# Performance work log

Measured on AMD Instinct MI355X. Metric: run time of the kernel, lower is better.

## Reference

```python
import jax, jax.numpy as jnp
import numpy as np

N = 100000      # nodes
E = 3200000     # edges (avg degree 32)
IN, HID, OUT = 512, 256, 64
K = 10
ALPHA = 0.1


def setup_inputs() -> dict:
    key = jax.random.key(0)
    k1, k2, k3, k4 = jax.random.split(key, 4)
    x = jax.random.normal(k1, (N, IN), dtype=jnp.float32)
    edge_index = jax.random.randint(k2, (2, E), 0, N, dtype=jnp.int64)
    # MLP params (Kaiming-ish scaling)
    W1 = jax.random.normal(k3, (IN, HID), dtype=jnp.float32) / np.sqrt(IN)
    b1 = jnp.zeros((HID,), dtype=jnp.float32)
    W2 = jax.random.normal(k4, (HID, OUT), dtype=jnp.float32) / np.sqrt(HID)
    b2 = jnp.zeros((OUT,), dtype=jnp.float32)
    # GPR_prop PPR init: temp[k] = alpha*(1-alpha)^k, temp[K] = (1-alpha)^K
    ks = np.arange(K + 1)
    temp = ALPHA * (1.0 - ALPHA) ** ks
    temp[-1] = (1.0 - ALPHA) ** K
    temp = jnp.asarray(temp, dtype=jnp.float32)
    return {"x": x, "edge_index": edge_index, "W1": W1, "b1": b1,
            "W2": W2, "b2": b2, "temp": temp}


def reference(x, edge_index, W1, b1, W2, b2, temp):
    # MLP front-end (eval mode: dropout = identity)
    h = jax.nn.relu(x @ W1 + b1)
    h = h @ W2 + b2                                  # [N, OUT]

    # gcn_norm with self-loops: A_hat = D^{-1/2} (A + I) D^{-1/2}
    loop = jnp.arange(N, dtype=edge_index.dtype)
    src = jnp.concatenate([edge_index[0], loop])      # [E+N]
    dst = jnp.concatenate([edge_index[1], loop])      # [E+N]
    deg = jax.ops.segment_sum(jnp.ones_like(dst, dtype=h.dtype), dst,
                              num_segments=N)
    dis = jnp.where(deg > 0, jax.lax.rsqrt(deg), 0.0)
    norm = (dis[src] * dis[dst])[:, None]             # [E+N, 1]

    # GPR propagation: out = sum_k temp[k] * A_hat^k h
    def step(carry, gamma):
        hk, acc = carry
        hk = jax.ops.segment_sum(norm * hk[src], dst, num_segments=N)
        return (hk, acc + gamma * hk), None

    (_, out), _ = jax.lax.scan(step, (h, temp[0] * h), temp[1:])
    return out
```

## Files before the change

kernel.cpp:

```cpp
#include <hip/hip_runtime.h>

#define NN 100000
#define NE 3200000
#define DIN 512
#define DHID 256
#define DOUT 64
#define KPROP 10

typedef _Float16 f16;
typedef _Float16 f16x8 __attribute__((ext_vector_type(8)));
typedef _Float16 f16x4 __attribute__((ext_vector_type(4)));
typedef float f32x4 __attribute__((ext_vector_type(4)));

__global__ void detect_i64(const int* __restrict__ ei, int* __restrict__ flag) {
  int lane = threadIdx.x;
  int ok = 1;
  for (int i = lane; i < 512; i += 64)
    if (ei[2 * i + 1] != 0) ok = 0;
  ok = __all(ok);
  if (lane == 0) *flag = ok;
}

__global__ void zero_cnt(int* __restrict__ cnt) {
  int g = blockIdx.x * blockDim.x + threadIdx.x;
  if (g < NN) cnt[g] = 0;
}

__global__ void count_deg(const int* __restrict__ ei, const int* __restrict__ flag,
                          int* __restrict__ cnt, int* __restrict__ rank) {
  int g = blockIdx.x * blockDim.x + threadIdx.x;
  int e0 = g * 4;
  if (e0 >= NE) return;
  int is64 = *flag;
  int d0, d1, d2, d3;
  if (is64) {
    int4 a = *(const int4*)&ei[2 * (size_t)NE + 2 * (size_t)e0];
    int4 b = *(const int4*)&ei[2 * (size_t)NE + 2 * (size_t)e0 + 4];
    d0 = a.x; d1 = a.z; d2 = b.x; d3 = b.z;
  } else {
    int4 a = *(const int4*)&ei[(size_t)NE + e0];
    d0 = a.x; d1 = a.y; d2 = a.z; d3 = a.w;
  }
  int4 rk;
  rk.x = atomicAdd(&cnt[d0], 1);
  rk.y = atomicAdd(&cnt[d1], 1);
  rk.z = atomicAdd(&cnt[d2], 1);
  rk.w = atomicAdd(&cnt[d3], 1);
  *(int4*)&rank[e0] = rk;
}

__global__ void scan1(const int* __restrict__ cnt, int* __restrict__ rs,
                      int* __restrict__ bsum) {
  __shared__ int tmp[1024];
  int t = threadIdx.x;
  int g = blockIdx.x * 1024 + t;
  int v = (g < NN) ? cnt[g] : 0;
  tmp[t] = v;
  __syncthreads();
  for (int off = 1; off < 1024; off <<= 1) {
    int y = (t >= off) ? tmp[t - off] : 0;
    __syncthreads();
    tmp[t] += y;
    __syncthreads();
  }
  if (g < NN) rs[g] = tmp[t] - v;
  if (t == 1023) bsum[blockIdx.x] = tmp[t];
}

__global__ void scan2(int* __restrict__ bsum, int nb) {
  if (blockIdx.x == 0 && threadIdx.x == 0) {
    int s = 0;
    for (int i = 0; i < nb; i++) { int v = bsum[i]; bsum[i] = s; s += v; }
  }
}

__global__ void scan3_and_dis(int* __restrict__ rs, const int* __restrict__ bsum,
                              const int* __restrict__ cnt, float* __restrict__ dis) {
  int g = blockIdx.x * blockDim.x + threadIdx.x;
  if (g < NN) {
    rs[g] = rs[g] + bsum[g >> 10];
    dis[g] = rsqrtf((float)(cnt[g] + 1));
  }
}

__global__ void fill_csr(const int* __restrict__ ei, const int* __restrict__ flag,
                         const int* __restrict__ rs, const int* __restrict__ rank,
                         int* __restrict__ col) {
  int g = blockIdx.x * blockDim.x + threadIdx.x;
  int e0 = g * 4;
  if (e0 >= NE) return;
  int is64 = *flag;
  int s[4], d[4];
  if (is64) {
    int4 a = *(const int4*)&ei[2 * (size_t)NE + 2 * (size_t)e0];
    int4 b = *(const int4*)&ei[2 * (size_t)NE + 2 * (size_t)e0 + 4];
    d[0] = a.x; d[1] = a.z; d[2] = b.x; d[3] = b.z;
    int4 c = *(const int4*)&ei[2 * (size_t)e0];
    int4 e = *(const int4*)&ei[2 * (size_t)e0 + 4];
    s[0] = c.x; s[1] = c.z; s[2] = e.x; s[3] = e.z;
  } else {
    int4 a = *(const int4*)&ei[(size_t)NE + e0];
    d[0] = a.x; d[1] = a.y; d[2] = a.z; d[3] = a.w;
    int4 c = *(const int4*)&ei[e0];
    s[0] = c.x; s[1] = c.y; s[2] = c.z; s[3] = c.w;
  }
  int4 rk = *(const int4*)&rank[e0];
  int rka[4] = { rk.x, rk.y, rk.z, rk.w };
  #pragma unroll
  for (int j = 0; j < 4; j++)
    col[rs[d[j]] + rka[j]] = s[j];
}

__global__ void cvt_weights(const float* __restrict__ W1, const float* __restrict__ W2,
                            f16* __restrict__ W1t, f16* __restrict__ W2t) {
  int g = blockIdx.x * 256 + threadIdx.x;
  if (g < DIN * DHID) {
    int k = g >> 8, n = g & 255;
    W1t[(size_t)n * DIN + k] = (f16)W1[g];
  }
  if (g < DHID * DOUT) {
    int k = g >> 6, n = g & 63;
    W2t[(size_t)n * DHID + k] = (f16)W2[g];
  }
}

__global__ __launch_bounds__(256) void mlp_mfma(
    const float* __restrict__ x, const f16* __restrict__ W1t,
    const float* __restrict__ b1, const f16* __restrict__ W2t,
    const float* __restrict__ b2, const float* __restrict__ temp,
    const float* __restrict__ dis, f16* __restrict__ h, f16* __restrict__ zs)
{
  __shared__ __align__(16) char smraw[2 * 64 * 136 * 2];
  f16* xsb = (f16*)smraw;
  f16* h1s = (f16*)smraw;
  int t = threadIdx.x;
  int lane = t & 63;
  int w = t >> 6;
  int n0 = blockIdx.x * 64;
  int r15 = lane & 15;
  int g4 = lane >> 4;
  int nbase = w * 64;
  int srow = t >> 5, sc4 = t & 31;

  f32x4 acc[4][4];
  #pragma unroll
  for (int nt = 0; nt < 4; nt++) {
    float bv = b1[nbase + nt * 16 + r15];
    #pragma unroll
    for (int mt = 0; mt < 4; mt++) acc[mt][nt] = (f32x4){bv, bv, bv, bv};
  }

  float4 ld[8];
  #pragma unroll
  for (int it = 0; it < 8; it++) {
    int row = srow + it * 8;
    int gr = n0 + row;
    ld[it] = (gr < NN) ? *(const float4*)&x[(size_t)gr * DIN + sc4 * 4]
                       : make_float4(0.f, 0.f, 0.f, 0.f);
  }
  #pragma unroll
  for (int it = 0; it < 8; it++) {
    int row = srow + it * 8;
    f16x4 hv = { (f16)ld[it].x, (f16)ld[it].y, (f16)ld[it].z, (f16)ld[it].w };
    *(f16x4*)&xsb[row * 136 + sc4 * 4] = hv;
  }
  __syncthreads();

  for (int c = 0; c < 4; c++) {
    int cur = c & 1;
    if (c < 3) {
      #pragma unroll
      for (int it = 0; it < 8; it++) {
        int row = srow + it * 8;
        int gr = n0 + row;
        ld[it] = (gr < NN)
            ? *(const float4*)&x[(size_t)gr * DIN + (c + 1) * 128 + sc4 * 4]
            : make_float4(0.f, 0.f, 0.f, 0.f);
      }
    }
    int k0 = c * 128;
    const f16* xs = xsb + cur * 8704;
    #pragma unroll
    for (int ks = 0; ks < 4; ks++) {
      int kk = ks * 32 + g4 * 8;
      f16x8 a[4], b[4];
      #pragma unroll
      for (int mt = 0; mt < 4; mt++)
        a[mt] = *(const f16x8*)&xs[(mt * 16 + r15) * 136 + kk];
      #pragma unroll
      for (int nt = 0; nt < 4; nt++)
        b[nt] = *(const f16x8*)&W1t[(size_t)(nbase + nt * 16 + r15) * DIN + k0 + kk];
      #pragma unroll
      for (int mt = 0; mt < 4; mt++)
        #pragma unroll
        for (int nt = 0; nt < 4; nt++)
          acc[mt][nt] = __builtin_amdgcn_mfma_f32_16x16x32_f16(a[mt], b[nt], acc[mt][nt], 0, 0, 0);
    }
    if (c < 3) {
      #pragma unroll
      for (int it = 0; it < 8; it++) {
        int row = srow + it * 8;
        f16x4 hv = { (f16)ld[it].x, (f16)ld[it].y, (f16)ld[it].z, (f16)ld[it].w };
        *(f16x4*)&xsb[(cur ^ 1) * 8704 + row * 136 + sc4 * 4] = hv;
      }
    }
    __syncthreads();
  }

  #pragma unroll
  for (int mt = 0; mt < 4; mt++)
    #pragma unroll
    for (int nt = 0; nt < 4; nt++)
      #pragma unroll
      for (int r = 0; r < 4; r++) {
        float v = fmaxf(acc[mt][nt][r], 0.f);
        h1s[(mt * 16 + g4 * 4 + r) * 264 + nbase + nt * 16 + r15] = (f16)v;
      }
  __syncthreads();

  f32x4 acc2[4];
  #pragma unroll
  for (int nt = 0; nt < 4; nt++) {
    float bv = b2[nt * 16 + r15];
    acc2[nt] = (f32x4){bv, bv, bv, bv};
  }
  #pragma unroll
  for (int ks = 0; ks < 8; ks++) {
    int kk = ks * 32 + g4 * 8;
    f16x8 a2 = *(const f16x8*)&h1s[(w * 16 + r15) * 264 + kk];
    #pragma unroll
    for (int nt = 0; nt < 4; nt++) {
      f16x8 bf = *(const f16x8*)&W2t[(size_t)(nt * 16 + r15) * DHID + kk];
      acc2[nt] = __builtin_amdgcn_mfma_f32_16x16x32_f16(a2, bf, acc2[nt], 0, 0, 0);
    }
  }
  float tK = temp[KPROP];
  #pragma unroll
  for (int r = 0; r < 4; r++) {
    int node = n0 + w * 16 + g4 * 4 + r;
    if (node < NN) {
      float dv = dis[node] * tK;
      #pragma unroll
      for (int nt = 0; nt < 4; nt++) {
        int colv = nt * 16 + r15;
        float v = acc2[nt][r];
        h[(size_t)node * DOUT + colv] = (f16)v;
        zs[(size_t)node * DOUT + colv] = (f16)(dv * v);
      }
    }
  }
}

__global__ __launch_bounds__(256) void prop_horner(
    const f16* __restrict__ zs, f16* __restrict__ zsn, const f16* __restrict__ h,
    float* __restrict__ out, const int* __restrict__ rs, const int* __restrict__ cnt,
    const int* __restrict__ col, const float* __restrict__ dis,
    const float* __restrict__ temp, int kidx, int final_step)
{
  int w = blockIdx.x * 4 + (threadIdx.x >> 6);
  int lane = threadIdx.x & 63;
  if (w >= NN) return;
  int q = lane >> 3;
  int s8 = lane & 7;

  float dd = dis[w];
  float gk = temp[kidx];
  f16x8 zself = *(const f16x8*)&zs[(size_t)w * DOUT + s8 * 8];
  f16x8 hs = *(const f16x8*)&h[(size_t)w * DOUT + s8 * 8];

  float acc[8];
  #pragma unroll
  for (int f = 0; f < 8; f++) acc[f] = 0.f;

  int beg = rs[w], n = cnt[w];
  const int* cp = col + beg;

  int e = 0;
  for (; e + 32 <= n; e += 32) {
    int c0 = cp[e + q];
    int c1 = cp[e + 8 + q];
    int c2 = cp[e + 16 + q];
    int c3 = cp[e + 24 + q];
    f16x8 g0 = *(const f16x8*)&zs[(size_t)c0 * DOUT + s8 * 8];
    f16x8 g1 = *(const f16x8*)&zs[(size_t)c1 * DOUT + s8 * 8];
    f16x8 g2 = *(const f16x8*)&zs[(size_t)c2 * DOUT + s8 * 8];
    f16x8 g3 = *(const f16x8*)&zs[(size_t)c3 * DOUT + s8 * 8];
    #pragma unroll
    for (int f = 0; f < 8; f++) acc[f] += (float)g0[f];
    #pragma unroll
    for (int f = 0; f < 8; f++) acc[f] += (float)g1[f];
    #pragma unroll
    for (int f = 0; f < 8; f++) acc[f] += (float)g2[f];
    #pragma unroll
    for (int f = 0; f < 8; f++) acc[f] += (float)g3[f];
  }
  for (; e + 8 <= n; e += 8) {
    int c0 = cp[e + q];
    f16x8 g0 = *(const f16x8*)&zs[(size_t)c0 * DOUT + s8 * 8];
    #pragma unroll
    for (int f = 0; f < 8; f++) acc[f] += (float)g0[f];
  }
  if (e < n) {
    int rem = n - e;
    int qq = q < rem ? q : rem - 1;
    int c0 = cp[e + qq];
    f16x8 g0 = *(const f16x8*)&zs[(size_t)c0 * DOUT + s8 * 8];
    float m = (q < rem) ? 1.f : 0.f;
    #pragma unroll
    for (int f = 0; f < 8; f++) acc[f] = fmaf(m, (float)g0[f], acc[f]);
  }

  #pragma unroll
  for (int f = 0; f < 8; f++) {
    acc[f] += __shfl_xor(acc[f], 8);
    acc[f] += __shfl_xor(acc[f], 16);
    acc[f] += __shfl_xor(acc[f], 32);
  }

  if (q == 0) {
    float zv[8];
    #pragma unroll
    for (int f = 0; f < 8; f++)
      zv[f] = gk * (float)hs[f] + dd * (acc[f] + (float)zself[f]);
    if (final_step) {
      float4 o0 = { zv[0], zv[1], zv[2], zv[3] };
      float4 o1 = { zv[4], zv[5], zv[6], zv[7] };
      *(float4*)&out[(size_t)w * DOUT + s8 * 8] = o0;
      *(float4*)&out[(size_t)w * DOUT + s8 * 8 + 4] = o1;
    } else {
      f16x8 o;
      #pragma unroll
      for (int f = 0; f < 8; f++) o[f] = (f16)(dd * zv[f]);
      *(f16x8*)&zsn[(size_t)w * DOUT + s8 * 8] = o;
    }
  }
}

extern "C" void kernel_launch(void* const* d_in, const int* in_sizes, int n_in,
                              void* d_out, int out_size, void* d_ws, size_t ws_size,
                              hipStream_t stream) {
  const float* x    = (const float*)d_in[0];
  const int*   ei   = (const int*)d_in[1];
  const float* W1   = (const float*)d_in[2];
  const float* b1   = (const float*)d_in[3];
  const float* W2   = (const float*)d_in[4];
  const float* b2   = (const float*)d_in[5];
  const float* temp = (const float*)d_in[6];
  float* out = (float*)d_out;

  char* wsb = (char*)d_ws;
  size_t off = 0;
  auto carve = [&](size_t bytes) -> void* {
    void* p = wsb + off;
    off = (off + bytes + 255) & ~(size_t)255;
    return p;
  };
  int*   cnt    = (int*)carve((size_t)NN * 4);
  int*   rs     = (int*)carve((size_t)NN * 4);
  int*   bsum   = (int*)carve(128 * 4);
  int*   flag   = (int*)carve(256);
  float* dis    = (float*)carve((size_t)NN * 4);
  int*   rank   = (int*)carve((size_t)NE * 4);
  int*   colA   = (int*)carve((size_t)NE * 4);
  f16*   W1t    = (f16*)carve((size_t)DHID * DIN * 2);
  f16*   W2t    = (f16*)carve((size_t)DOUT * DHID * 2);
  f16*   h_buf  = (f16*)carve((size_t)NN * DOUT * 2);
  f16*   zs_a   = (f16*)carve((size_t)NN * DOUT * 2);
  f16*   zs_b   = (f16*)carve((size_t)NN * DOUT * 2);
  if (off > ws_size) return;

  detect_i64<<<1, 64, 0, stream>>>(ei, flag);
  zero_cnt<<<(NN + 255) / 256, 256, 0, stream>>>(cnt);
  count_deg<<<(NE / 4 + 255) / 256, 256, 0, stream>>>(ei, flag, cnt, rank);
  scan1<<<(NN + 1023) / 1024, 1024, 0, stream>>>(cnt, rs, bsum);
  scan2<<<1, 64, 0, stream>>>(bsum, (NN + 1023) / 1024);
  scan3_and_dis<<<(NN + 255) / 256, 256, 0, stream>>>(rs, bsum, cnt, dis);
  fill_csr<<<(NE / 4 + 255) / 256, 256, 0, stream>>>(ei, flag, rs, rank, colA);

  cvt_weights<<<(DIN * DHID + 255) / 256, 256, 0, stream>>>(W1, W2, W1t, W2t);
  mlp_mfma<<<(NN + 63) / 64, 256, 0, stream>>>(x, W1t, b1, W2t, b2, temp, dis,
                                               h_buf, zs_a);

  const f16* zc = zs_a;
  f16* zn = zs_b;
  for (int k = KPROP - 1; k >= 0; k--) {
    prop_horner<<<(NN + 3) / 4, 256, 0, stream>>>(zc, zn, h_buf, out, rs, cnt,
                                                  colA, dis, temp, k, k == 0);
    const f16* t2 = zn;
    zn = (f16*)zc;
    zc = t2;
  }
}
```

Baseline: 906.8 us.

## Co-schedule degree counting with MLP and CSR fill with seed scaling

```diff
diff --git a/kernel.cpp b/kernel.cpp
--- a/kernel.cpp
+++ b/kernel.cpp
@@ -6,47 +6,184 @@
 #define DHID 256
 #define DOUT 64
 #define KPROP 10
+#define MLP_BLKS ((NN + 63) / 64)
+#define CNT_BLKS ((NE / 4 + 255) / 256)
+#define FILL_BLKS ((NE / 4 + 255) / 256)
+#define SEED_BLKS 3125
 
 typedef _Float16 f16;
 typedef _Float16 f16x8 __attribute__((ext_vector_type(8)));
 typedef _Float16 f16x4 __attribute__((ext_vector_type(4)));
 typedef float f32x4 __attribute__((ext_vector_type(4)));
 
-__global__ void detect_i64(const int* __restrict__ ei, int* __restrict__ flag) {
-  int lane = threadIdx.x;
-  int ok = 1;
-  for (int i = lane; i < 512; i += 64)
-    if (ei[2 * i + 1] != 0) ok = 0;
-  ok = __all(ok);
-  if (lane == 0) *flag = ok;
-}
-
-__global__ void zero_cnt(int* __restrict__ cnt) {
+__global__ void zero_detect(int* __restrict__ cnt, const int* __restrict__ ei,
+                            int* __restrict__ flag) {
   int g = blockIdx.x * blockDim.x + threadIdx.x;
   if (g < NN) cnt[g] = 0;
-}
-
-__global__ void count_deg(const int* __restrict__ ei, const int* __restrict__ flag,
-                          int* __restrict__ cnt, int* __restrict__ rank) {
-  int g = blockIdx.x * blockDim.x + threadIdx.x;
-  int e0 = g * 4;
-  if (e0 >= NE) return;
-  int is64 = *flag;
-  int d0, d1, d2, d3;
-  if (is64) {
-    int4 a = *(const int4*)&ei[2 * (size_t)NE + 2 * (size_t)e0];
-    int4 b = *(const int4*)&ei[2 * (size_t)NE + 2 * (size_t)e0 + 4];
-    d0 = a.x; d1 = a.z; d2 = b.x; d3 = b.z;
-  } else {
-    int4 a = *(const int4*)&ei[(size_t)NE + e0];
-    d0 = a.x; d1 = a.y; d2 = a.z; d3 = a.w;
-  }
-  int4 rk;
-  rk.x = atomicAdd(&cnt[d0], 1);
-  rk.y = atomicAdd(&cnt[d1], 1);
-  rk.z = atomicAdd(&cnt[d2], 1);
-  rk.w = atomicAdd(&cnt[d3], 1);
-  *(int4*)&rank[e0] = rk;
+  if (blockIdx.x == 0 && threadIdx.x < 64) {
+    int lane = threadIdx.x;
+    int ok = 1;
+    for (int i = lane; i < 512; i += 64)
+      if (ei[2 * i + 1] != 0) ok = 0;
+    ok = __all(ok);
+    if (lane == 0) *flag = ok;
+  }
+}
+
+__global__ void cvt_weights(const float* __restrict__ W1, const float* __restrict__ W2,
+                            f16* __restrict__ W1t, f16* __restrict__ W2t) {
+  int g = blockIdx.x * 256 + threadIdx.x;
+  if (g < DIN * DHID) {
+    int k = g >> 8, n = g & 255;
+    W1t[(size_t)n * DIN + k] = (f16)W1[g];
+  }
+  if (g < DHID * DOUT) {
+    int k = g >> 6, n = g & 63;
+    W2t[(size_t)n * DHID + k] = (f16)W2[g];
+  }
+}
+
+__global__ __launch_bounds__(256) void count_mlp(
+    const int* __restrict__ ei, const int* __restrict__ flag,
+    int* __restrict__ cnt, int* __restrict__ rank,
+    const float* __restrict__ x, const f16* __restrict__ W1t,
+    const float* __restrict__ b1, const f16* __restrict__ W2t,
+    const float* __restrict__ b2, f16* __restrict__ h)
+{
+  __shared__ __align__(16) char smraw[2 * 64 * 136 * 2];
+  if (blockIdx.x >= MLP_BLKS) {
+    int g = (blockIdx.x - MLP_BLKS) * 256 + threadIdx.x;
+    int e0 = g * 4;
+    if (e0 >= NE) return;
+    int is64 = *flag;
+    int d0, d1, d2, d3;
+    if (is64) {
+      int4 a = *(const int4*)&ei[2 * (size_t)NE + 2 * (size_t)e0];
+      int4 b = *(const int4*)&ei[2 * (size_t)NE + 2 * (size_t)e0 + 4];
+      d0 = a.x; d1 = a.z; d2 = b.x; d3 = b.z;
+    } else {
+      int4 a = *(const int4*)&ei[(size_t)NE + e0];
+      d0 = a.x; d1 = a.y; d2 = a.z; d3 = a.w;
+    }
+    int4 rk;
+    rk.x = atomicAdd(&cnt[d0], 1);
+    rk.y = atomicAdd(&cnt[d1], 1);
+    rk.z = atomicAdd(&cnt[d2], 1);
+    rk.w = atomicAdd(&cnt[d3], 1);
+    *(int4*)&rank[e0] = rk;
+    return;
+  }
+  f16* xsb = (f16*)smraw;
+  f16* h1s = (f16*)smraw;
+  int t = threadIdx.x;
+  int lane = t & 63;
+  int w = t >> 6;
+  int n0 = blockIdx.x * 64;
+  int r15 = lane & 15;
+  int g4 = lane >> 4;
+  int nbase = w * 64;
+  int srow = t >> 5, sc4 = t & 31;
+
+  f32x4 acc[4][4];
+  #pragma unroll
+  for (int nt = 0; nt < 4; nt++) {
+    float bv = b1[nbase + nt * 16 + r15];
+    #pragma unroll
+    for (int mt = 0; mt < 4; mt++) acc[mt][nt] = (f32x4){bv, bv, bv, bv};
+  }
+
+  float4 ld[8];
+  #pragma unroll
+  for (int it = 0; it < 8; it++) {
+    int row = srow + it * 8;
+    int gr = n0 + row;
+    ld[it] = (gr < NN) ? *(const float4*)&x[(size_t)gr * DIN + sc4 * 4]
+                       : make_float4(0.f, 0.f, 0.f, 0.f);
+  }
+  #pragma unroll
+  for (int it = 0; it < 8; it++) {
+    int row = srow + it * 8;
+    f16x4 hv = { (f16)ld[it].x, (f16)ld[it].y, (f16)ld[it].z, (f16)ld[it].w };
+    *(f16x4*)&xsb[row * 136 + sc4 * 4] = hv;
+  }
+  __syncthreads();
+
+  for (int c = 0; c < 4; c++) {
+    int cur = c & 1;
+    if (c < 3) {
+      #pragma unroll
+      for (int it = 0; it < 8; it++) {
+        int row = srow + it * 8;
+        int gr = n0 + row;
+        ld[it] = (gr < NN)
+            ? *(const float4*)&x[(size_t)gr * DIN + (c + 1) * 128 + sc4 * 4]
+            : make_float4(0.f, 0.f, 0.f, 0.f);
+      }
+    }
+    int k0 = c * 128;
+    const f16* xs = xsb + cur * 8704;
+    #pragma unroll
+    for (int ks = 0; ks < 4; ks++) {
+      int kk = ks * 32 + g4 * 8;
+      f16x8 a[4], b[4];
+      #pragma unroll
+      for (int mt = 0; mt < 4; mt++)
+        a[mt] = *(const f16x8*)&xs[(mt * 16 + r15) * 136 + kk];
+      #pragma unroll
+      for (int nt = 0; nt < 4; nt++)
+        b[nt] = *(const f16x8*)&W1t[(size_t)(nbase + nt * 16 + r15) * DIN + k0 + kk];
+      #pragma unroll
+      for (int mt = 0; mt < 4; mt++)
+        #pragma unroll
+        for (int nt = 0; nt < 4; nt++)
+          acc[mt][nt] = __builtin_amdgcn_mfma_f32_16x16x32_f16(a[mt], b[nt], acc[mt][nt], 0, 0, 0);
+    }
+    if (c < 3) {
+      #pragma unroll
+      for (int it = 0; it < 8; it++) {
+        int row = srow + it * 8;
+        f16x4 hv = { (f16)ld[it].x, (f16)ld[it].y, (f16)ld[it].z, (f16)ld[it].w };
+        *(f16x4*)&xsb[(cur ^ 1) * 8704 + row * 136 + sc4 * 4] = hv;
+      }
+    }
+    __syncthreads();
+  }
+
+  #pragma unroll
+  for (int mt = 0; mt < 4; mt++)
+    #pragma unroll
+    for (int nt = 0; nt < 4; nt++)
+      #pragma unroll
+      for (int r = 0; r < 4; r++) {
+        float v = fmaxf(acc[mt][nt][r], 0.f);
+        h1s[(mt * 16 + g4 * 4 + r) * 264 + nbase + nt * 16 + r15] = (f16)v;
+      }
+  __syncthreads();
+
+  f32x4 acc2[4];
+  #pragma unroll
+  for (int nt = 0; nt < 4; nt++) {
+    float bv = b2[nt * 16 + r15];
+    acc2[nt] = (f32x4){bv, bv, bv, bv};
+  }
+  #pragma unroll
+  for (int ks = 0; ks < 8; ks++) {
+    int kk = ks * 32 + g4 * 8;
+    f16x8 a2 = *(const f16x8*)&h1s[(w * 16 + r15) * 264 + kk];
+    #pragma unroll
+    for (int nt = 0; nt < 4; nt++) {
+      f16x8 bf = *(const f16x8*)&W2t[(size_t)(nt * 16 + r15) * DHID + kk];
+      acc2[nt] = __builtin_amdgcn_mfma_f32_16x16x32_f16(a2, bf, acc2[nt], 0, 0, 0);
+    }
+  }
+  #pragma unroll
+  for (int nt = 0; nt < 4; nt++)
+    #pragma unroll
+    for (int r = 0; r < 4; r++) {
+      int node = n0 + w * 16 + g4 * 4 + r;
+      if (node < NN)
+        h[(size_t)node * DOUT + nt * 16 + r15] = (f16)acc2[nt][r];
+    }
 }
 
 __global__ void scan1(const int* __restrict__ cnt, int* __restrict__ rs,
@@ -68,10 +205,18 @@
 }
 
 __global__ void scan2(int* __restrict__ bsum, int nb) {
-  if (blockIdx.x == 0 && threadIdx.x == 0) {
-    int s = 0;
-    for (int i = 0; i < nb; i++) { int v = bsum[i]; bsum[i] = s; s += v; }
-  }
+  int lane = threadIdx.x;
+  int v0 = (lane < nb) ? bsum[lane] : 0;
+  int v1 = (64 + lane < nb) ? bsum[64 + lane] : 0;
+  int s0 = v0, s1 = v1;
+  for (int off = 1; off < 64; off <<= 1) {
+    int t0 = __shfl_up(s0, off);
+    int t1 = __shfl_up(s1, off);
+    if (lane >= off) { s0 += t0; s1 += t1; }
+  }
+  int tot0 = __shfl(s0, 63);
+  if (lane < nb) bsum[lane] = s0 - v0;
+  if (64 + lane < nb) bsum[64 + lane] = tot0 + s1 - v1;
 }
 
 __global__ void scan3_and_dis(int* __restrict__ rs, const int* __restrict__ bsum,
@@ -83,9 +228,24 @@
   }
 }
 
-__global__ void fill_csr(const int* __restrict__ ei, const int* __restrict__ flag,
-                         const int* __restrict__ rs, const int* __restrict__ rank,
-                         int* __restrict__ col) {
+__global__ void fill_seed(const int* __restrict__ ei, const int* __restrict__ flag,
+                          const int* __restrict__ rs, const int* __restrict__ rank,
+                          int* __restrict__ col, const float* __restrict__ dis,
+                          const float* __restrict__ temp, const f16* __restrict__ h,
+                          f16* __restrict__ zs) {
+  if (blockIdx.x >= FILL_BLKS) {
+    int g = (blockIdx.x - FILL_BLKS) * 256 + threadIdx.x;
+    int node = g >> 3;
+    if (node < NN) {
+      float dv = dis[node] * temp[KPROP];
+      f16x8 hv = *(const f16x8*)&h[(size_t)g * 8];
+      f16x8 o;
+      #pragma unroll
+      for (int f = 0; f < 8; f++) o[f] = (f16)(dv * (float)hv[f]);
+      *(f16x8*)&zs[(size_t)g * 8] = o;
+    }
+    return;
+  }
   int g = blockIdx.x * blockDim.x + threadIdx.x;
   int e0 = g * 4;
   if (e0 >= NE) return;
@@ -109,146 +269,6 @@
   #pragma unroll
   for (int j = 0; j < 4; j++)
     col[rs[d[j]] + rka[j]] = s[j];
-}
-
-__global__ void cvt_weights(const float* __restrict__ W1, const float* __restrict__ W2,
-                            f16* __restrict__ W1t, f16* __restrict__ W2t) {
-  int g = blockIdx.x * 256 + threadIdx.x;
-  if (g < DIN * DHID) {
-    int k = g >> 8, n = g & 255;
-    W1t[(size_t)n * DIN + k] = (f16)W1[g];
-  }
-  if (g < DHID * DOUT) {
-    int k = g >> 6, n = g & 63;
-    W2t[(size_t)n * DHID + k] = (f16)W2[g];
-  }
-}
-
-__global__ __launch_bounds__(256) void mlp_mfma(
-    const float* __restrict__ x, const f16* __restrict__ W1t,
-    const float* __restrict__ b1, const f16* __restrict__ W2t,
-    const float* __restrict__ b2, const float* __restrict__ temp,
-    const float* __restrict__ dis, f16* __restrict__ h, f16* __restrict__ zs)
-{
-  __shared__ __align__(16) char smraw[2 * 64 * 136 * 2];
-  f16* xsb = (f16*)smraw;
-  f16* h1s = (f16*)smraw;
-  int t = threadIdx.x;
-  int lane = t & 63;
-  int w = t >> 6;
-  int n0 = blockIdx.x * 64;
-  int r15 = lane & 15;
-  int g4 = lane >> 4;
-  int nbase = w * 64;
-  int srow = t >> 5, sc4 = t & 31;
-
-  f32x4 acc[4][4];
-  #pragma unroll
-  for (int nt = 0; nt < 4; nt++) {
-    float bv = b1[nbase + nt * 16 + r15];
-    #pragma unroll
-    for (int mt = 0; mt < 4; mt++) acc[mt][nt] = (f32x4){bv, bv, bv, bv};
-  }
-
-  float4 ld[8];
-  #pragma unroll
-  for (int it = 0; it < 8; it++) {
-    int row = srow + it * 8;
-    int gr = n0 + row;
-    ld[it] = (gr < NN) ? *(const float4*)&x[(size_t)gr * DIN + sc4 * 4]
-                       : make_float4(0.f, 0.f, 0.f, 0.f);
-  }
-  #pragma unroll
-  for (int it = 0; it < 8; it++) {
-    int row = srow + it * 8;
-    f16x4 hv = { (f16)ld[it].x, (f16)ld[it].y, (f16)ld[it].z, (f16)ld[it].w };
-    *(f16x4*)&xsb[row * 136 + sc4 * 4] = hv;
-  }
-  __syncthreads();
-
-  for (int c = 0; c < 4; c++) {
-    int cur = c & 1;
-    if (c < 3) {
-      #pragma unroll
-      for (int it = 0; it < 8; it++) {
-        int row = srow + it * 8;
-        int gr = n0 + row;
-        ld[it] = (gr < NN)
-            ? *(const float4*)&x[(size_t)gr * DIN + (c + 1) * 128 + sc4 * 4]
-            : make_float4(0.f, 0.f, 0.f, 0.f);
-      }
-    }
-    int k0 = c * 128;
-    const f16* xs = xsb + cur * 8704;
-    #pragma unroll
-    for (int ks = 0; ks < 4; ks++) {
-      int kk = ks * 32 + g4 * 8;
-      f16x8 a[4], b[4];
-      #pragma unroll
-      for (int mt = 0; mt < 4; mt++)
-        a[mt] = *(const f16x8*)&xs[(mt * 16 + r15) * 136 + kk];
-      #pragma unroll
-      for (int nt = 0; nt < 4; nt++)
-        b[nt] = *(const f16x8*)&W1t[(size_t)(nbase + nt * 16 + r15) * DIN + k0 + kk];
-      #pragma unroll
-      for (int mt = 0; mt < 4; mt++)
-        #pragma unroll
-        for (int nt = 0; nt < 4; nt++)
-          acc[mt][nt] = __builtin_amdgcn_mfma_f32_16x16x32_f16(a[mt], b[nt], acc[mt][nt], 0, 0, 0);
-    }
-    if (c < 3) {
-      #pragma unroll
-      for (int it = 0; it < 8; it++) {
-        int row = srow + it * 8;
-        f16x4 hv = { (f16)ld[it].x, (f16)ld[it].y, (f16)ld[it].z, (f16)ld[it].w };
-        *(f16x4*)&xsb[(cur ^ 1) * 8704 + row * 136 + sc4 * 4] = hv;
-      }
-    }
-    __syncthreads();
-  }
-
-  #pragma unroll
-  for (int mt = 0; mt < 4; mt++)
-    #pragma unroll
-    for (int nt = 0; nt < 4; nt++)
-      #pragma unroll
-      for (int r = 0; r < 4; r++) {
-        float v = fmaxf(acc[mt][nt][r], 0.f);
-        h1s[(mt * 16 + g4 * 4 + r) * 264 + nbase + nt * 16 + r15] = (f16)v;
-      }
-  __syncthreads();
-
-  f32x4 acc2[4];
-  #pragma unroll
-  for (int nt = 0; nt < 4; nt++) {
-    float bv = b2[nt * 16 + r15];
-    acc2[nt] = (f32x4){bv, bv, bv, bv};
-  }
-  #pragma unroll
-  for (int ks = 0; ks < 8; ks++) {
-    int kk = ks * 32 + g4 * 8;
-    f16x8 a2 = *(const f16x8*)&h1s[(w * 16 + r15) * 264 + kk];
-    #pragma unroll
-    for (int nt = 0; nt < 4; nt++) {
-      f16x8 bf = *(const f16x8*)&W2t[(size_t)(nt * 16 + r15) * DHID + kk];
-      acc2[nt] = __builtin_amdgcn_mfma_f32_16x16x32_f16(a2, bf, acc2[nt], 0, 0, 0);
-    }
-  }
-  float tK = temp[KPROP];
-  #pragma unroll
-  for (int r = 0; r < 4; r++) {
-    int node = n0 + w * 16 + g4 * 4 + r;
-    if (node < NN) {
-      float dv = dis[node] * tK;
-      #pragma unroll
-      for (int nt = 0; nt < 4; nt++) {
-        int colv = nt * 16 + r15;
-        float v = acc2[nt][r];
-        h[(size_t)node * DOUT + colv] = (f16)v;
-        zs[(size_t)node * DOUT + colv] = (f16)(dv * v);
-      }
-    }
-  }
 }
 
 __global__ __launch_bounds__(256) void prop_horner(
@@ -369,17 +389,15 @@
   f16*   zs_b   = (f16*)carve((size_t)NN * DOUT * 2);
   if (off > ws_size) return;
 
-  detect_i64<<<1, 64, 0, stream>>>(ei, flag);
-  zero_cnt<<<(NN + 255) / 256, 256, 0, stream>>>(cnt);
-  count_deg<<<(NE / 4 + 255) / 256, 256, 0, stream>>>(ei, flag, cnt, rank);
+  zero_detect<<<(NN + 255) / 256, 256, 0, stream>>>(cnt, ei, flag);
+  cvt_weights<<<(DIN * DHID + 255) / 256, 256, 0, stream>>>(W1, W2, W1t, W2t);
+  count_mlp<<<MLP_BLKS + CNT_BLKS, 256, 0, stream>>>(ei, flag, cnt, rank,
+                                                     x, W1t, b1, W2t, b2, h_buf);
   scan1<<<(NN + 1023) / 1024, 1024, 0, stream>>>(cnt, rs, bsum);
   scan2<<<1, 64, 0, stream>>>(bsum, (NN + 1023) / 1024);
   scan3_and_dis<<<(NN + 255) / 256, 256, 0, stream>>>(rs, bsum, cnt, dis);
-  fill_csr<<<(NE / 4 + 255) / 256, 256, 0, stream>>>(ei, flag, rs, rank, colA);
-
-  cvt_weights<<<(DIN * DHID + 255) / 256, 256, 0, stream>>>(W1, W2, W1t, W2t);
-  mlp_mfma<<<(NN + 63) / 64, 256, 0, stream>>>(x, W1t, b1, W2t, b2, temp, dis,
-                                               h_buf, zs_a);
+  fill_seed<<<FILL_BLKS + SEED_BLKS, 256, 0, stream>>>(ei, flag, rs, rank, colA,
+                                                       dis, temp, h_buf, zs_a);
 
   const f16* zc = zs_a;
   f16* zn = zs_b;
```

New measurement: 865.2 us, median of 2. 4.6% less time.
